# Kernel optimization log

Measured on AMD Instinct MI355X. Metric: run time of the kernel, lower is better.

The kernel has to match this reference:

```python
import jax, jax.numpy as jnp
import numpy as np

N_NODES = 50000
N_EDGES = 1600000
IN_C, HID_C, OUT_C = 64, 64, 7


def setup_inputs() -> dict:
    key = jax.random.key(0)
    ks = jax.random.split(key, 8)
    x = jax.random.normal(ks[0], (N_NODES, IN_C), dtype=jnp.float32)
    edge_index = jax.random.randint(ks[1], (2, N_EDGES), 0, N_NODES, dtype=jnp.int64)
    s_in = 1.0 / np.sqrt(IN_C)
    s_hid = 1.0 / np.sqrt(HID_C)
    W1 = jax.random.normal(ks[2], (HID_C, IN_C), dtype=jnp.float32) * s_in
    b1 = jnp.zeros((HID_C,), dtype=jnp.float32)
    W2 = jax.random.normal(ks[3], (HID_C, HID_C), dtype=jnp.float32) * s_hid
    b2 = jnp.zeros((HID_C,), dtype=jnp.float32)
    W3 = jax.random.normal(ks[4], (OUT_C, HID_C), dtype=jnp.float32) * s_hid
    b3 = jnp.zeros((OUT_C,), dtype=jnp.float32)
    return {"x": x, "edge_index": edge_index, "W1": W1, "b1": b1,
            "W2": W2, "b2": b2, "W3": W3, "b3": b3}


def _gcn_conv(x, src, dst, W, b):
    # GCNConv(normalize=False): lin -> sum-aggregate over incoming edges -> +bias
    h = x @ W.T                                   # [N, out]
    msg = h[src]                                  # gather source features [E, out]
    agg = jax.ops.segment_sum(msg, dst, num_segments=N_NODES)  # scatter-add
    return agg + b


def reference(x, edge_index, W1, b1, W2, b2, W3, b3):
    src, dst = edge_index[0], edge_index[1]
    h = jax.nn.relu(_gcn_conv(x, src, dst, W1, b1))   # dropout is identity in eval
    h = jax.nn.relu(_gcn_conv(h, src, dst, W2, b2))
    h = _gcn_conv(h, src, dst, W3, b3)
    return jax.nn.log_softmax(h, axis=-1)
```

## Files before the change

### kernel.cpp

```cpp
#include <hip/hip_runtime.h>
#include <math.h>

#define N_NODES 50000
#define N_EDGES 1600000
#define C 64
#define OUTC 7

#define NB 196
#define BCAP 10240
#define CHUNK 8192

__device__ __forceinline__ unsigned int pk_bf16(float a, float b) {
    unsigned int ua = __float_as_uint(a);
    ua = (ua + 0x7FFFu + ((ua >> 16) & 1u)) >> 16;
    unsigned int ub = __float_as_uint(b);
    ub = (ub + 0x7FFFu + ((ub >> 16) & 1u)) >> 16;
    return ua | (ub << 16);
}

__global__ __launch_bounds__(256) void bin_kernel(const int* __restrict__ src,
                                                  const int* __restrict__ dst,
                                                  unsigned int* __restrict__ buckets,
                                                  int* __restrict__ gcursor) {
    __shared__ unsigned int staged[CHUNK];
    __shared__ int hist[NB], scanb[NB], cur[NB], baseb[NB];
    const int tid = threadIdx.x;
    const int base = blockIdx.x * CHUNK;
    int n = N_EDGES - base; if (n > CHUNK) n = CHUNK;

    for (int b = tid; b < NB; b += 256) { hist[b] = 0; cur[b] = 0; }
    __syncthreads();

    const int4* src4 = (const int4*)(src + base);
    const int4* dst4 = (const int4*)(dst + base);
    unsigned int v[32];
    int nv = n >> 2;
#pragma unroll
    for (int k = 0; k < 8; ++k) {
        int i4 = k * 256 + tid;
        if (i4 < nv) {
            int4 s4 = src4[i4];
            int4 d4 = dst4[i4];
            unsigned int d0 = (unsigned int)d4.x, d1 = (unsigned int)d4.y;
            unsigned int d2 = (unsigned int)d4.z, d3 = (unsigned int)d4.w;
            v[k * 4 + 0] = (d0 << 16) | (unsigned int)s4.x;
            v[k * 4 + 1] = (d1 << 16) | (unsigned int)s4.y;
            v[k * 4 + 2] = (d2 << 16) | (unsigned int)s4.z;
            v[k * 4 + 3] = (d3 << 16) | (unsigned int)s4.w;
            atomicAdd(&hist[d0 >> 8], 1);
            atomicAdd(&hist[d1 >> 8], 1);
            atomicAdd(&hist[d2 >> 8], 1);
            atomicAdd(&hist[d3 >> 8], 1);
        }
    }
    __syncthreads();
    if (tid == 0) {
        int run = 0;
        for (int b = 0; b < NB; ++b) { scanb[b] = run; run += hist[b]; }
    }
    __syncthreads();
#pragma unroll
    for (int k = 0; k < 8; ++k) {
        int i4 = k * 256 + tid;
        if (i4 < nv) {
#pragma unroll
            for (int q = 0; q < 4; ++q) {
                unsigned int w = v[k * 4 + q];
                int b = w >> 24;
                int p = scanb[b] + atomicAdd(&cur[b], 1);
                staged[p] = w;
            }
        }
    }
    __syncthreads();
    if (tid < NB) baseb[tid] = atomicAdd(&gcursor[tid], hist[tid]);
    __syncthreads();
    for (int i = tid; i < n; i += 256) {
        unsigned int w = staged[i];
        int b = w >> 24;
        buckets[(size_t)b * BCAP + baseb[b] + (i - scanb[b])] = w;
    }
}

__global__ __launch_bounds__(256) void build_csr(const unsigned int* __restrict__ buckets,
                                                 const int* __restrict__ gcursor,
                                                 unsigned int* __restrict__ csr,
                                                 int* __restrict__ off) {
    __shared__ int hist[256], part[256], offx[256], cur[256];
    __shared__ int gl[NB];
    __shared__ int s_cnt, s_base;
    const int tid = threadIdx.x;
    const int b = blockIdx.x;

    hist[tid] = 0;
    cur[tid] = 0;
    if (tid < NB) gl[tid] = gcursor[tid];
    __syncthreads();
    if (tid == 0) {
        int bs = 0;
        for (int i = 0; i < b; ++i) bs += gl[i];
        s_base = bs;
        s_cnt = gl[b];
    }
    __syncthreads();
    const int cnt = s_cnt;
    const int gbase = s_base;
    const unsigned int* bk = buckets + (size_t)b * BCAP;

    for (int i = tid; i < cnt; i += 256) {
        atomicAdd(&hist[(bk[i] >> 16) & 255], 1);
    }
    __syncthreads();
    part[tid] = hist[tid];
    __syncthreads();
    for (int d = 1; d < 256; d <<= 1) {
        int t = (tid >= d) ? part[tid - d] : 0;
        __syncthreads();
        part[tid] += t;
        __syncthreads();
    }
    offx[tid] = (tid == 0) ? 0 : part[tid - 1];
    __syncthreads();
    int node = b * 256 + tid;
    if (node < N_NODES) off[node] = gbase + offx[tid];
    if (b == NB - 1 && tid == 0) off[N_NODES] = gbase + cnt;
    for (int i = tid; i < cnt; i += 256) {
        unsigned int w = bk[i];
        int dl = (w >> 16) & 255;
        int p = offx[dl] + atomicAdd(&cur[dl], 1);
        csr[gbase + p] = w & 0xFFFFu;
    }
}


__global__ __launch_bounds__(256) void linear64_x(const float* __restrict__ x,
                                                  const float* __restrict__ W,
                                                  unsigned int* __restrict__ tb) {
    const int cg = blockIdx.x & 3;
    const int r = (blockIdx.x >> 2) * 256 + threadIdx.x;
    if (r >= N_NODES) return;
    float4 xr[16];
    const float4* xp = (const float4*)(x + (size_t)r * 64);
#pragma unroll
    for (int j = 0; j < 16; ++j) xr[j] = xp[j];
    const float* xf = (const float*)xr;

    const float* Wp = W + cg * 16 * 64;
    unsigned int* orow = tb + (size_t)r * 32 + cg * 8;
    for (int c0 = 0; c0 < 16; c0 += 8) {
        float acc[8] = {0.f, 0.f, 0.f, 0.f, 0.f, 0.f, 0.f, 0.f};
#pragma unroll
        for (int k = 0; k < 64; ++k) {
            float xv = xf[k];
#pragma unroll
            for (int j = 0; j < 8; ++j)
                acc[j] += xv * Wp[(c0 + j) * 64 + k];
        }
        uint4 w;
        w.x = pk_bf16(acc[0], acc[1]);
        w.y = pk_bf16(acc[2], acc[3]);
        w.z = pk_bf16(acc[4], acc[5]);
        w.w = pk_bf16(acc[6], acc[7]);
        ((uint4*)orow)[c0 >> 3] = w;
    }
}

__global__ __launch_bounds__(256) void linear64_h(const unsigned int* __restrict__ hb,
                                                  const float* __restrict__ W,
                                                  unsigned int* __restrict__ tb) {
    const int cg = blockIdx.x & 3;
    const int r = (blockIdx.x >> 2) * 256 + threadIdx.x;
    if (r >= N_NODES) return;
    float xf[64];
    const uint4* hp = (const uint4*)(hb + (size_t)r * 32);
#pragma unroll
    for (int j = 0; j < 8; ++j) {
        uint4 u = hp[j];
        xf[j * 8 + 0] = __uint_as_float(u.x << 16);
        xf[j * 8 + 1] = __uint_as_float(u.x & 0xFFFF0000u);
        xf[j * 8 + 2] = __uint_as_float(u.y << 16);
        xf[j * 8 + 3] = __uint_as_float(u.y & 0xFFFF0000u);
        xf[j * 8 + 4] = __uint_as_float(u.z << 16);
        xf[j * 8 + 5] = __uint_as_float(u.z & 0xFFFF0000u);
        xf[j * 8 + 6] = __uint_as_float(u.w << 16);
        xf[j * 8 + 7] = __uint_as_float(u.w & 0xFFFF0000u);
    }

    const float* Wp = W + cg * 16 * 64;
    unsigned int* orow = tb + (size_t)r * 32 + cg * 8;
    for (int c0 = 0; c0 < 16; c0 += 8) {
        float acc[8] = {0.f, 0.f, 0.f, 0.f, 0.f, 0.f, 0.f, 0.f};
#pragma unroll
        for (int k = 0; k < 64; ++k) {
            float xv = xf[k];
#pragma unroll
            for (int j = 0; j < 8; ++j)
                acc[j] += xv * Wp[(c0 + j) * 64 + k];
        }
        uint4 w;
        w.x = pk_bf16(acc[0], acc[1]);
        w.y = pk_bf16(acc[2], acc[3]);
        w.z = pk_bf16(acc[4], acc[5]);
        w.w = pk_bf16(acc[6], acc[7]);
        ((uint4*)orow)[c0 >> 3] = w;
    }
}

__global__ __launch_bounds__(128) void linear7_h(const unsigned int* __restrict__ hb,
                                                 const float* __restrict__ W,
                                                 unsigned int* __restrict__ out) {
    int r = blockIdx.x * 128 + threadIdx.x;
    if (r >= N_NODES) return;
    float xf[64];
    const uint4* hp = (const uint4*)(hb + (size_t)r * 32);
#pragma unroll
    for (int j = 0; j < 8; ++j) {
        uint4 u = hp[j];
        xf[j * 8 + 0] = __uint_as_float(u.x << 16);
        xf[j * 8 + 1] = __uint_as_float(u.x & 0xFFFF0000u);
        xf[j * 8 + 2] = __uint_as_float(u.y << 16);
        xf[j * 8 + 3] = __uint_as_float(u.y & 0xFFFF0000u);
        xf[j * 8 + 4] = __uint_as_float(u.z << 16);
        xf[j * 8 + 5] = __uint_as_float(u.z & 0xFFFF0000u);
        xf[j * 8 + 6] = __uint_as_float(u.w << 16);
        xf[j * 8 + 7] = __uint_as_float(u.w & 0xFFFF0000u);
    }

    float acc[7] = {0.f, 0.f, 0.f, 0.f, 0.f, 0.f, 0.f};
#pragma unroll
    for (int k = 0; k < 64; ++k) {
        float xv = xf[k];
#pragma unroll
        for (int j = 0; j < 7; ++j)
            acc[j] += xv * W[j * 64 + k];
    }
    uint4 w;
    w.x = pk_bf16(acc[0], acc[1]);
    w.y = pk_bf16(acc[2], acc[3]);
    w.z = pk_bf16(acc[4], acc[5]);
    w.w = pk_bf16(acc[6], 0.f);
    ((uint4*)(out + (size_t)r * 4))[0] = w;
}


__global__ __launch_bounds__(256) void gather64b(const int* __restrict__ off,
                                                 const unsigned int* __restrict__ csr_src,
                                                 const unsigned int* __restrict__ tb,
                                                 const float* __restrict__ b,
                                                 unsigned int* __restrict__ hb) {
    int node = blockIdx.x * 4 + (threadIdx.x >> 6);
    if (node >= N_NODES) return;
    const int lane = threadIdx.x & 63;
    const int slot = lane >> 3;
    const int ch8  = lane & 7;
    int e0 = off[node], e1 = off[node + 1];
    const uint4* t4 = (const uint4*)tb;
    float s[8] = {0.f, 0.f, 0.f, 0.f, 0.f, 0.f, 0.f, 0.f};
    for (int e = e0; e < e1; e += 16) {
        int i0 = e + slot;
        int i1 = e + 8 + slot;
        bool p0 = i0 < e1, p1 = i1 < e1;
        unsigned int a0 = csr_src[p0 ? i0 : e];
        unsigned int a1 = csr_src[p1 ? i1 : e];
        uint4 v0 = t4[(size_t)a0 * 8 + ch8];
        uint4 v1 = t4[(size_t)a1 * 8 + ch8];
        if (p0) {
            s[0] += __uint_as_float(v0.x << 16);
            s[1] += __uint_as_float(v0.x & 0xFFFF0000u);
            s[2] += __uint_as_float(v0.y << 16);
            s[3] += __uint_as_float(v0.y & 0xFFFF0000u);
            s[4] += __uint_as_float(v0.z << 16);
            s[5] += __uint_as_float(v0.z & 0xFFFF0000u);
            s[6] += __uint_as_float(v0.w << 16);
            s[7] += __uint_as_float(v0.w & 0xFFFF0000u);
        }
        if (p1) {
            s[0] += __uint_as_float(v1.x << 16);
            s[1] += __uint_as_float(v1.x & 0xFFFF0000u);
            s[2] += __uint_as_float(v1.y << 16);
            s[3] += __uint_as_float(v1.y & 0xFFFF0000u);
            s[4] += __uint_as_float(v1.z << 16);
            s[5] += __uint_as_float(v1.z & 0xFFFF0000u);
            s[6] += __uint_as_float(v1.w << 16);
            s[7] += __uint_as_float(v1.w & 0xFFFF0000u);
        }
    }
#pragma unroll
    for (int d = 8; d <= 32; d <<= 1) {
#pragma unroll
        for (int j = 0; j < 8; ++j) s[j] += __shfl_xor(s[j], d, 64);
    }
    if (lane < 8) {
        const float4 b0 = ((const float4*)b)[ch8 * 2];
        const float4 b1 = ((const float4*)b)[ch8 * 2 + 1];
        float r0 = fmaxf(s[0] + b0.x, 0.f);
        float r1 = fmaxf(s[1] + b0.y, 0.f);
        float r2 = fmaxf(s[2] + b0.z, 0.f);
        float r3 = fmaxf(s[3] + b0.w, 0.f);
        float r4 = fmaxf(s[4] + b1.x, 0.f);
        float r5 = fmaxf(s[5] + b1.y, 0.f);
        float r6 = fmaxf(s[6] + b1.z, 0.f);
        float r7 = fmaxf(s[7] + b1.w, 0.f);
        uint4 w;
        w.x = pk_bf16(r0, r1);
        w.y = pk_bf16(r2, r3);
        w.z = pk_bf16(r4, r5);
        w.w = pk_bf16(r6, r7);
        ((uint4*)(hb + (size_t)node * 32))[ch8] = w;
    }
}

__global__ __launch_bounds__(256) void gather7_lsm(const int* __restrict__ off,
                                                   const unsigned int* __restrict__ csr_src,
                                                   const unsigned int* __restrict__ t3,
                                                   const float* __restrict__ b,
                                                   float* __restrict__ out) {
    int node = blockIdx.x * 4 + (threadIdx.x >> 6);
    if (node >= N_NODES) return;
    const int lane = threadIdx.x & 63;
    const int slot = lane >> 1;
    const int h    = lane & 1;
    int e0 = off[node], e1 = off[node + 1];
    const uint2* t2 = (const uint2*)t3;
    float sx = 0.f, sy = 0.f, sz = 0.f, sw = 0.f;
    for (int e = e0 + slot; e < e1; e += 32) {
        unsigned int s = csr_src[e];
        uint2 v = t2[(size_t)s * 2 + h];
        sx += __uint_as_float(v.x << 16);
        sy += __uint_as_float(v.x & 0xFFFF0000u);
        sz += __uint_as_float(v.y << 16);
        sw += __uint_as_float(v.y & 0xFFFF0000u);
    }
#pragma unroll
    for (int d = 2; d <= 32; d <<= 1) {
        sx += __shfl_xor(sx, d, 64); sy += __shfl_xor(sy, d, 64);
        sz += __shfl_xor(sz, d, 64); sw += __shfl_xor(sw, d, 64);
    }
    float z0 = sx + b[h * 4 + 0];
    float z1 = sy + b[h * 4 + 1];
    float z2 = sz + b[h * 4 + 2];
    float z3 = (h == 0) ? (sw + b[3]) : -1e30f;
    float m = fmaxf(fmaxf(z0, z1), fmaxf(z2, z3));
    m = fmaxf(m, __shfl_xor(m, 1, 64));
    float ex = __expf(z0 - m) + __expf(z1 - m) + __expf(z2 - m) + __expf(z3 - m);
    ex += __shfl_xor(ex, 1, 64);
    float l = m + __logf(ex);
    if (lane < 2) {
        float* o = out + (size_t)node * 7 + h * 4;
        o[0] = z0 - l; o[1] = z1 - l; o[2] = z2 - l;
        if (h == 0) o[3] = z3 - l;
    }
}

extern "C" void kernel_launch(void* const* d_in, const int* in_sizes, int n_in,
                              void* d_out, int out_size, void* d_ws, size_t ws_size,
                              hipStream_t stream) {
    const float* x  = (const float*)d_in[0];
    const int*   ei = (const int*)d_in[1];
    const float* W1 = (const float*)d_in[2];
    const float* b1 = (const float*)d_in[3];
    const float* W2 = (const float*)d_in[4];
    const float* b2 = (const float*)d_in[5];
    const float* W3 = (const float*)d_in[6];
    const float* b3 = (const float*)d_in[7];
    float* out = (float*)d_out;

    const int* src = ei;
    const int* dst = ei + N_EDGES;

    float* A = (float*)d_ws;
    float* B = A + (size_t)N_NODES * C;
    unsigned int* csr = (unsigned int*)(B + (size_t)N_NODES * C);
    int* off     = (int*)(csr + N_EDGES);
    int* gcursor = off + N_NODES + 8;
    unsigned int* buckets = (unsigned int*)A;
    unsigned int* Abf     = (unsigned int*)A;
    unsigned int* Hbf     = (unsigned int*)B;

    const int l64grid = ((N_NODES + 255) / 256) * 4;
    const int l7grid  = (N_NODES + 127) / 128;
    const int ngrid   = (N_NODES + 3) / 4;

    (void)hipMemsetAsync(gcursor, 0, NB * sizeof(int), stream);
    bin_kernel<<<(N_EDGES + CHUNK - 1) / CHUNK, 256, 0, stream>>>(src, dst, buckets, gcursor);
    build_csr<<<NB, 256, 0, stream>>>(buckets, gcursor, csr, off);

    linear64_x<<<l64grid, 256, 0, stream>>>(x, W1, Abf);
    gather64b<<<ngrid, 256, 0, stream>>>(off, csr, Abf, b1, Hbf);

    linear64_h<<<l64grid, 256, 0, stream>>>(Hbf, W2, Abf);
    gather64b<<<ngrid, 256, 0, stream>>>(off, csr, Abf, b2, Hbf);

    linear7_h<<<l7grid, 128, 0, stream>>>(Hbf, W3, Abf);
    gather7_lsm<<<ngrid, 256, 0, stream>>>(off, csr, Abf, b3, out);
}
```

Before: 259.4 us.

## Use bf16 MFMA for the 64-wide linear layers with pre-packed inputs

Replaces the per-thread scalar FP32 dot-product kernels for the two 64x64 linear layers with one wave-level kernel built on mfma_f32_16x16x32_bf16. Weights and the input features x are first converted to packed bf16 by new small pack kernels, so the first layer now reads bf16 instead of fp32. The aim is to cut ALU time and the repeated reads of each row across four column-group blocks. In exchange it adds three extra launches, an extra pass over x, lower precision on the first layer's inputs and weights, and narrow 4-byte strided output stores after lane shuffles.

New measurement: 232.4 us. -10.4%, faster.

```diff
diff --git a/kernel.cpp b/kernel.cpp
--- a/kernel.cpp
+++ b/kernel.cpp
@@ -9,6 +9,9 @@
 #define NB 196
 #define BCAP 10240
 #define CHUNK 8192
+
+typedef __attribute__((ext_vector_type(8))) short bf16x8;
+typedef __attribute__((ext_vector_type(4))) float f32x4;
 
 __device__ __forceinline__ unsigned int pk_bf16(float a, float b) {
     unsigned int ua = __float_as_uint(a);
@@ -17,6 +20,8 @@
     ub = (ub + 0x7FFFu + ((ub >> 16) & 1u)) >> 16;
     return ua | (ub << 16);
 }
+
+union U4B8 { uint4 u; bf16x8 s; };
 
 __global__ __launch_bounds__(256) void bin_kernel(const int* __restrict__ src,
                                                   const int* __restrict__ dst,
@@ -133,43 +138,75 @@
 }
 
 
-__global__ __launch_bounds__(256) void linear64_x(const float* __restrict__ x,
-                                                  const float* __restrict__ W,
-                                                  unsigned int* __restrict__ tb) {
-    const int cg = blockIdx.x & 3;
-    const int r = (blockIdx.x >> 2) * 256 + threadIdx.x;
-    if (r >= N_NODES) return;
-    float4 xr[16];
-    const float4* xp = (const float4*)(x + (size_t)r * 64);
-#pragma unroll
-    for (int j = 0; j < 16; ++j) xr[j] = xp[j];
-    const float* xf = (const float*)xr;
-
-    const float* Wp = W + cg * 16 * 64;
-    unsigned int* orow = tb + (size_t)r * 32 + cg * 8;
-    for (int c0 = 0; c0 < 16; c0 += 8) {
-        float acc[8] = {0.f, 0.f, 0.f, 0.f, 0.f, 0.f, 0.f, 0.f};
-#pragma unroll
-        for (int k = 0; k < 64; ++k) {
-            float xv = xf[k];
-#pragma unroll
-            for (int j = 0; j < 8; ++j)
-                acc[j] += xv * Wp[(c0 + j) * 64 + k];
-        }
-        uint4 w;
-        w.x = pk_bf16(acc[0], acc[1]);
-        w.y = pk_bf16(acc[2], acc[3]);
-        w.z = pk_bf16(acc[4], acc[5]);
-        w.w = pk_bf16(acc[6], acc[7]);
-        ((uint4*)orow)[c0 >> 3] = w;
-    }
-}
-
-__global__ __launch_bounds__(256) void linear64_h(const unsigned int* __restrict__ hb,
-                                                  const float* __restrict__ W,
-                                                  unsigned int* __restrict__ tb) {
-    const int cg = blockIdx.x & 3;
-    const int r = (blockIdx.x >> 2) * 256 + threadIdx.x;
+__global__ __launch_bounds__(256) void pack_x(const float* __restrict__ x,
+                                              unsigned int* __restrict__ xb) {
+    int idx = blockIdx.x * 256 + threadIdx.x;
+    if (idx >= N_NODES * 32) return;
+    const float2* x2 = (const float2*)x;
+    float2 v = x2[idx];
+    xb[idx] = pk_bf16(v.x, v.y);
+}
+
+__global__ __launch_bounds__(256) void pack_w(const float* __restrict__ W,
+                                              unsigned int* __restrict__ Wb) {
+    int idx = blockIdx.x * 256 + threadIdx.x;
+    if (idx >= 64 * 32) return;
+    const float2* w2 = (const float2*)W;
+    float2 v = w2[idx];
+    Wb[idx] = pk_bf16(v.x, v.y);
+}
+
+__global__ __launch_bounds__(256) void linear64_mfma(const unsigned int* __restrict__ in,
+                                                     const unsigned int* __restrict__ Wb,
+                                                     unsigned int* __restrict__ out) {
+    const int wave = threadIdx.x >> 6;
+    const int lane = threadIdx.x & 63;
+    const int quad = lane >> 4;
+    const int l16  = lane & 15;
+    const int rbase = blockIdx.x * 64 + wave * 16;
+    if (rbase >= N_NODES) return;
+
+    U4B8 bfrag[4][2];
+#pragma unroll
+    for (int ct = 0; ct < 4; ++ct)
+#pragma unroll
+        for (int kt = 0; kt < 2; ++kt)
+            bfrag[ct][kt].u = *(const uint4*)(Wb + (ct * 16 + l16) * 32 + kt * 16 + quad * 4);
+
+    U4B8 afrag[2];
+#pragma unroll
+    for (int kt = 0; kt < 2; ++kt)
+        afrag[kt].u = *(const uint4*)(in + (size_t)(rbase + l16) * 32 + kt * 16 + quad * 4);
+
+    f32x4 acc[4];
+#pragma unroll
+    for (int ct = 0; ct < 4; ++ct) {
+        f32x4 z = {0.f, 0.f, 0.f, 0.f};
+        z = __builtin_amdgcn_mfma_f32_16x16x32_bf16(afrag[0].s, bfrag[ct][0].s, z, 0, 0, 0);
+        z = __builtin_amdgcn_mfma_f32_16x16x32_bf16(afrag[1].s, bfrag[ct][1].s, z, 0, 0, 0);
+        acc[ct] = z;
+    }
+
+    const int colp = l16 >> 1;
+    const bool even = (l16 & 1) == 0;
+#pragma unroll
+    for (int ct = 0; ct < 4; ++ct) {
+#pragma unroll
+        for (int i = 0; i < 4; ++i) {
+            float v = acc[ct][i];
+            float p = __shfl_xor(v, 1, 64);
+            if (even) {
+                int row = rbase + quad * 4 + i;
+                out[(size_t)row * 32 + ct * 8 + colp] = pk_bf16(v, p);
+            }
+        }
+    }
+}
+
+__global__ __launch_bounds__(128) void linear7_h(const unsigned int* __restrict__ hb,
+                                                 const float* __restrict__ W,
+                                                 unsigned int* __restrict__ out) {
+    int r = blockIdx.x * 128 + threadIdx.x;
     if (r >= N_NODES) return;
     float xf[64];
     const uint4* hp = (const uint4*)(hb + (size_t)r * 32);
@@ -186,46 +223,6 @@
         xf[j * 8 + 7] = __uint_as_float(u.w & 0xFFFF0000u);
     }
 
-    const float* Wp = W + cg * 16 * 64;
-    unsigned int* orow = tb + (size_t)r * 32 + cg * 8;
-    for (int c0 = 0; c0 < 16; c0 += 8) {
-        float acc[8] = {0.f, 0.f, 0.f, 0.f, 0.f, 0.f, 0.f, 0.f};
-#pragma unroll
-        for (int k = 0; k < 64; ++k) {
-            float xv = xf[k];
-#pragma unroll
-            for (int j = 0; j < 8; ++j)
-                acc[j] += xv * Wp[(c0 + j) * 64 + k];
-        }
-        uint4 w;
-        w.x = pk_bf16(acc[0], acc[1]);
-        w.y = pk_bf16(acc[2], acc[3]);
-        w.z = pk_bf16(acc[4], acc[5]);
-        w.w = pk_bf16(acc[6], acc[7]);
-        ((uint4*)orow)[c0 >> 3] = w;
-    }
-}
-
-__global__ __launch_bounds__(128) void linear7_h(const unsigned int* __restrict__ hb,
-                                                 const float* __restrict__ W,
-                                                 unsigned int* __restrict__ out) {
-    int r = blockIdx.x * 128 + threadIdx.x;
-    if (r >= N_NODES) return;
-    float xf[64];
-    const uint4* hp = (const uint4*)(hb + (size_t)r * 32);
-#pragma unroll
-    for (int j = 0; j < 8; ++j) {
-        uint4 u = hp[j];
-        xf[j * 8 + 0] = __uint_as_float(u.x << 16);
-        xf[j * 8 + 1] = __uint_as_float(u.x & 0xFFFF0000u);
-        xf[j * 8 + 2] = __uint_as_float(u.y << 16);
-        xf[j * 8 + 3] = __uint_as_float(u.y & 0xFFFF0000u);
-        xf[j * 8 + 4] = __uint_as_float(u.z << 16);
-        xf[j * 8 + 5] = __uint_as_float(u.z & 0xFFFF0000u);
-        xf[j * 8 + 6] = __uint_as_float(u.w << 16);
-        xf[j * 8 + 7] = __uint_as_float(u.w & 0xFFFF0000u);
-    }
-
     float acc[7] = {0.f, 0.f, 0.f, 0.f, 0.f, 0.f, 0.f};
 #pragma unroll
     for (int k = 0; k < 64; ++k) {
@@ -241,7 +238,6 @@
     w.w = pk_bf16(acc[6], 0.f);
     ((uint4*)(out + (size_t)r * 4))[0] = w;
 }
-
 
 __global__ __launch_bounds__(256) void gather64b(const int* __restrict__ off,
                                                  const unsigned int* __restrict__ csr_src,
@@ -373,22 +369,29 @@
     unsigned int* csr = (unsigned int*)(B + (size_t)N_NODES * C);
     int* off     = (int*)(csr + N_EDGES);
     int* gcursor = off + N_NODES + 8;
+    unsigned int* Wb1 = (unsigned int*)(gcursor + 256);
+    unsigned int* Wb2 = Wb1 + 2048;
     unsigned int* buckets = (unsigned int*)A;
     unsigned int* Abf     = (unsigned int*)A;
     unsigned int* Hbf     = (unsigned int*)B;
-
-    const int l64grid = ((N_NODES + 255) / 256) * 4;
-    const int l7grid  = (N_NODES + 127) / 128;
-    const int ngrid   = (N_NODES + 3) / 4;
+    unsigned int* xb      = (unsigned int*)B + (size_t)N_NODES * 32;
+
+    const int mfmagrid = (N_NODES + 63) / 64;
+    const int l7grid   = (N_NODES + 127) / 128;
+    const int ngrid    = (N_NODES + 3) / 4;
+
+    pack_w<<<8, 256, 0, stream>>>(W1, Wb1);
+    pack_w<<<8, 256, 0, stream>>>(W2, Wb2);
+    pack_x<<<(N_NODES * 32 + 255) / 256, 256, 0, stream>>>(x, xb);
 
     (void)hipMemsetAsync(gcursor, 0, NB * sizeof(int), stream);
     bin_kernel<<<(N_EDGES + CHUNK - 1) / CHUNK, 256, 0, stream>>>(src, dst, buckets, gcursor);
     build_csr<<<NB, 256, 0, stream>>>(buckets, gcursor, csr, off);
 
-    linear64_x<<<l64grid, 256, 0, stream>>>(x, W1, Abf);
+    linear64_mfma<<<mfmagrid, 256, 0, stream>>>(xb, Wb1, Abf);
     gather64b<<<ngrid, 256, 0, stream>>>(off, csr, Abf, b1, Hbf);
 
-    linear64_h<<<l64grid, 256, 0, stream>>>(Hbf, W2, Abf);
+    linear64_mfma<<<mfmagrid, 256, 0, stream>>>(Hbf, Wb2, Abf);
     gather64b<<<ngrid, 256, 0, stream>>>(off, csr, Abf, b2, Hbf);
 
     linear7_h<<<l7grid, 128, 0, stream>>>(Hbf, W3, Abf);
```
